# Performance work log

Hardware: AMD Instinct MI355X
Metric: run time of the kernel (lower is better)

## Reference

```python
import jax, jax.numpy as jnp
import numpy as np

B, T, D = 32, 2048, 512


def setup_inputs() -> dict:
    key = jax.random.key(0)
    x = jax.random.normal(key, (B, T, D), dtype=jnp.float32)
    return {"x": x}


def reference(x):
    """DmvCell RNN with aggregations ('mean','var','max').

    Active partials: count, sum, max, mean, sn (Welford M2), var.
    Per step t:
        count += 1
        sum   += x_t
        max    = maximum(max, x_t)
        prev_mean = mean; mean = sum / count
        sn    += (x_t - prev_mean) * (x_t - mean)
        var    = sn / count
        out_t  = concat([mean, var, max])
    Initial states are zeros (Keras default). Returns the full output
    sequence [B, T, 3*D].
    """
    b, t, d = x.shape
    dt = x.dtype

    def step(carry, xt):
        count, s, mx, mean, sn = carry
        count = count + jnp.asarray(1, dt)          # [B,1]
        s = s + xt                                   # [B,D]
        mx = jnp.maximum(mx, xt)                     # [B,D]
        prev_mean = mean
        mean = s / count                             # [B,D]
        sn = sn + (xt - prev_mean) * (xt - mean)     # [B,D]
        var = sn / count                             # [B,D]
        out = jnp.concatenate([mean, var, mx], axis=-1)  # [B,3D]
        return (count, s, mx, mean, sn), out

    init = (
        jnp.zeros((b, 1), dt),   # count
        jnp.zeros((b, d), dt),   # sum
        jnp.zeros((b, d), dt),   # max
        jnp.zeros((b, d), dt),   # mean
        jnp.zeros((b, d), dt),   # sn
    )
    _, ys = jax.lax.scan(step, init, jnp.swapaxes(x, 0, 1))  # ys: [T,B,3D]
    return jnp.swapaxes(ys, 0, 1)  # [B,T,3D]
```

## Files before the change

kernel.cpp:

```cpp
#include <hip/hip_runtime.h>


#define BB 32
#define TT 2048
#define DD 512
#define NCHAIN (BB * DD)

typedef float f32x4 __attribute__((ext_vector_type(4)));

__device__ __forceinline__ float fast_rcp(float x) {
#if __has_builtin(__builtin_amdgcn_rcpf)
    return __builtin_amdgcn_rcpf(x);
#else
    return 1.0f / x;
#endif
}

__device__ __forceinline__ f32x4 vmax4(f32x4 a, f32x4 b) {
#if __has_builtin(__builtin_elementwise_max)
    return __builtin_elementwise_max(a, b);
#else
    f32x4 r;
    r.x = fmaxf(a.x, b.x); r.y = fmaxf(a.y, b.y);
    r.z = fmaxf(a.z, b.z); r.w = fmaxf(a.w, b.w);
    return r;
#endif
}

__device__ __forceinline__ void nts(f32x4 v, float* p) {
#if __has_builtin(__builtin_nontemporal_store)
    __builtin_nontemporal_store(v, (f32x4*)p);
#else
    *(f32x4*)p = v;
#endif
}

struct St1 {
    float n;
    f32x4 s, m2, mx;
};

__device__ __forceinline__ void st1_zero(St1& r) {
    r.n = 0.f;
    r.s = r.m2 = r.mx = (f32x4){0.f, 0.f, 0.f, 0.f};
}

__device__ __forceinline__ void st1_merge(St1& r, float tn, float itn,
                                          f32x4 ts, f32x4 tm, f32x4 tx) {
    if (r.n == 0.f) {
        r.n = tn; r.s = ts; r.m2 = tm; r.mx = tx;
    } else {
        float n     = r.n + tn;
        float irn   = fast_rcp(r.n);
        float scale = r.n * tn * fast_rcp(n);
        f32x4 da = ts * itn - r.s * irn;
        r.m2 += tm + da * da * scale;
        r.s += ts;
        r.mx = vmax4(r.mx, tx);
        r.n = n;
    }
}

template <int NC>
__launch_bounds__(256)
__global__ void dmv_agg_kernel(const float* __restrict__ x,
                               f32x4* __restrict__ ws4) {
    constexpr int CHUNK = TT / NC;
    f32x4* __restrict__ aS  = ws4;
    f32x4* __restrict__ aM2 = ws4 + (size_t)NC * 4096;
    f32x4* __restrict__ aMX = ws4 + 2 * (size_t)NC * 4096;

    const int tid = blockIdx.x * 256 + threadIdx.x;
    const int W   = tid >> 6;
    const int l   = tid & 63;
    const int c   = W & (NC - 1);
    const int b   = W / NC;

    const float* xp = x + ((size_t)(b * TT + c * CHUNK)) * DD + 4 * l;

    f32x4 s0 = {0,0,0,0}, s1 = {0,0,0,0};
    f32x4 q0 = {0,0,0,0}, q1 = {0,0,0,0};
    f32x4 m0 = {0,0,0,0}, m1 = {0,0,0,0};
    #pragma unroll 4
    for (int k = 0; k < CHUNK; ++k) {
        f32x4 a  = *(const f32x4*)(xp + (size_t)k * DD);
        f32x4 b2 = *(const f32x4*)(xp + (size_t)k * DD + 256);
        s0 += a;  q0 += a * a;   m0 = vmax4(m0, a);
        s1 += b2; q1 += b2 * b2; m1 = vmax4(m1, b2);
    }
    const size_t o = (size_t)c * 4096 + (size_t)b * 128 + l;
    const float ic = 1.0f / (float)CHUNK;
    aS[o]       = s0;  aS[o + 64]  = s1;
    aM2[o]      = q0 - s0 * s0 * ic;
    aM2[o + 64] = q1 - s1 * s1 * ic;
    aMX[o]      = m0;  aMX[o + 64] = m1;
}

template <int NC>
__launch_bounds__(512)
__global__ void dmv_scan_split(const float* __restrict__ x,
                               const f32x4* __restrict__ ws4,
                               float* __restrict__ out) {
    constexpr int CHUNK = TT / NC;
    constexpr int GRP   = NC / 4;
    const f32x4* __restrict__ aS  = ws4;
    const f32x4* __restrict__ aM2 = ws4 + (size_t)NC * 4096;
    const f32x4* __restrict__ aMX = ws4 + 2 * (size_t)NC * 4096;

    __shared__ f32x4 part[8][3][64];

    const int tid = threadIdx.x;
    const int w   = tid >> 6;
    const int l   = tid & 63;
    const int h   = w & 1;
    const int cw  = w >> 1;
    const int g   = blockIdx.x & (GRP - 1);
    const int b   = blockIdx.x / GRP;
    const int c0  = g * 4;
    const int c   = c0 + cw;

    constexpr float icf = 1.0f / (float)CHUNK;
    const int hofs = 64 * h;

    St1 q; st1_zero(q);
    for (int j = cw * g; j < (cw + 1) * g; ++j) {
        const size_t oj = (size_t)j * 4096 + (size_t)b * 128 + l + hofs;
        st1_merge(q, (float)CHUNK, icf, aS[oj], aM2[oj], aMX[oj]);
    }
    part[w][0][l] = q.s; part[w][1][l] = q.m2; part[w][2][l] = q.mx;
    __syncthreads();

    St1 r; st1_zero(r);
    if (g > 0) {
        const float qn  = (float)(g * CHUNK);
        const float iqn = fast_rcp(qn);
        #pragma unroll
        for (int qq = 0; qq < 4; ++qq) {
            const int pw = 2 * qq + h;
            st1_merge(r, qn, iqn, part[pw][0][l], part[pw][1][l], part[pw][2][l]);
        }
    }
    for (int j = c0; j < c; ++j) {
        const size_t oj = (size_t)j * 4096 + (size_t)b * 128 + l + hofs;
        st1_merge(r, (float)CHUNK, icf, aS[oj], aM2[oj], aMX[oj]);
    }

    float cnt = r.n;
    f32x4 rs = r.s, rm2 = r.m2, rmx = r.mx;
    f32x4 rmean = {0,0,0,0};
    if (c > 0) rmean = rs * fast_rcp(cnt);

    const float* xp = x   + ((size_t)(b * TT + c * CHUNK)) * DD + h * 256 + 4 * l;
    float*       op = out + ((size_t)(b * TT + c * CHUNK)) * (3 * DD) + h * 256 + 4 * l;

    #pragma unroll 4
    for (int k = 0; k < CHUNK; ++k) {
        f32x4 v = *(const f32x4*)(xp + (size_t)k * DD);
        cnt += 1.f;
        float inv = fast_rcp(cnt);
        rs += v;
        rmx = vmax4(rmx, v);
        f32x4 nm = rs * inv;
        rm2 += (v - rmean) * (v - nm);
        rmean = nm;
        f32x4 var = rm2 * inv;
        float* row = op + (size_t)k * (3 * DD);
        nts(nm,  row);
        nts(var, row + 512);
        nts(rmx, row + 1024);
    }
}

#define FNW 16
#define FCHUNK (TT / FNW)
#define DGRP 64

__launch_bounds__(1024, 1)
__global__ void dmv_scan_fallback(const float* __restrict__ x,
                                  float* __restrict__ out) {
    __shared__ float aggS[FNW][DGRP];
    __shared__ float aggM2[FNW][DGRP];
    __shared__ float aggMX[FNW][DGRP];

    const int tid = threadIdx.x;
    const int w   = tid >> 6;
    const int l   = tid & 63;
    const int b   = blockIdx.x >> 3;
    const int d0  = (blockIdx.x & 7) * DGRP;

    const float* xp = x   + ((size_t)b * TT) * DD + d0 + l
                          + (size_t)(w * FCHUNK) * DD;
    float*       op = out + ((size_t)b * TT) * (3 * DD) + d0 + l
                          + (size_t)(w * FCHUNK) * (3 * DD);

    if (w < FNW - 1) {
        float s = 0.f, ss = 0.f, mx = 0.f;
        #pragma unroll 8
        for (int k = 0; k < FCHUNK; ++k) {
            float xv = xp[(size_t)k * DD];
            s += xv; ss = fmaf(xv, xv, ss); mx = fmaxf(mx, xv);
        }
        aggS[w][l] = s;
        aggM2[w][l] = ss - s * s * (1.0f / FCHUNK);
        aggMX[w][l] = mx;
    }
    __syncthreads();

    float c_n = 0.f, c_s = 0.f, c_m2 = 0.f, c_mx = 0.f;
    for (int j = 0; j < w; ++j) {
        float bs = aggS[j][l], bm2 = aggM2[j][l], bmx = aggMX[j][l];
        if (j == 0) {
            c_n = (float)FCHUNK; c_s = bs; c_m2 = bm2; c_mx = bmx;
        } else {
            float n  = c_n + (float)FCHUNK;
            float da = bs * (1.0f / FCHUNK) - c_s / c_n;
            c_m2 = c_m2 + bm2 + da * da * (c_n * (float)FCHUNK / n);
            c_s += bs; c_mx = fmaxf(c_mx, bmx); c_n = n;
        }
    }

    float cnt = c_n, rs = c_s, rm2 = c_m2, rmx = c_mx;
    float rmean = (w > 0) ? rs / cnt : 0.f;
    #pragma unroll 8
    for (int k = 0; k < FCHUNK; ++k) {
        float xv = xp[(size_t)k * DD];
        cnt += 1.f;
        float inv = fast_rcp(cnt);
        rs += xv; rmx = fmaxf(rmx, xv);
        float nm = rs * inv;
        rm2 += (xv - rmean) * (xv - nm);
        rmean = nm;
        float var = rm2 * inv;
        float* orow = op + (size_t)k * (3 * DD);
        orow[0] = nm; orow[DD] = var; orow[2 * DD] = rmx;
    }
}

template <int NC>
static void launch_2k(const float* x, float* out, void* d_ws, hipStream_t stream) {
    dmv_agg_kernel<NC><<<dim3(8 * NC), dim3(256), 0, stream>>>(x, (f32x4*)d_ws);
    dmv_scan_split<NC><<<dim3(8 * NC), dim3(512), 0, stream>>>(
        x, (const f32x4*)d_ws, out);
}

extern "C" void kernel_launch(void* const* d_in, const int* in_sizes, int n_in,
                              void* d_out, int out_size, void* d_ws, size_t ws_size,
                              hipStream_t stream) {
    (void)in_sizes; (void)n_in; (void)out_size;
    const float* x = (const float*)d_in[0];
    float* out = (float*)d_out;

    const size_t need64 = (size_t)3 * 64 * 4096 * sizeof(f32x4);
    const size_t need32 = (size_t)3 * 32 * 4096 * sizeof(f32x4);

    if (d_ws && ws_size >= need64) {
        launch_2k<64>(x, out, d_ws, stream);
    } else if (d_ws && ws_size >= need32) {
        launch_2k<32>(x, out, d_ws, stream);
    } else {
        dmv_scan_fallback<<<dim3(BB * (DD / DGRP)), dim3(1024), 0, stream>>>(x, out);
    }
}
```

Before: 118.9 us.

## Fuse aggregate and scan kernels using per-batch atomic counters in cooperative launch

```diff
diff --git a/kernel.cpp b/kernel.cpp
--- a/kernel.cpp
+++ b/kernel.cpp
@@ -5,6 +5,7 @@
 #define TT 2048
 #define DD 512
 #define NCHAIN (BB * DD)
+#define NAGG 128
 
 typedef float f32x4 __attribute__((ext_vector_type(4)));
 
@@ -35,10 +36,7 @@
 #endif
 }
 
-struct St1 {
-    float n;
-    f32x4 s, m2, mx;
-};
+struct St1 { float n; f32x4 s, m2, mx; };
 
 __device__ __forceinline__ void st1_zero(St1& r) {
     r.n = 0.f;
@@ -58,6 +56,125 @@
         r.s += ts;
         r.mx = vmax4(r.mx, tx);
         r.n = n;
+    }
+}
+
+template <int NC>
+__launch_bounds__(256, 6)
+__global__ void dmv_fused(const float* __restrict__ x,
+                          f32x4* __restrict__ ws4,
+                          int* __restrict__ cnt,
+                          float* __restrict__ out) {
+    constexpr int CHUNK = TT / NC;
+    constexpr int GRP   = NC / 4;
+    f32x4* __restrict__ aS  = ws4;
+    f32x4* __restrict__ aM2 = ws4 + (size_t)NC * 4096;
+    f32x4* __restrict__ aMX = ws4 + 2 * (size_t)NC * 4096;
+    constexpr float icf = 1.0f / (float)CHUNK;
+
+    __shared__ f32x4 part[4][3][64];
+
+    const int tid = threadIdx.x;
+    const int w   = tid >> 6;
+    const int l   = tid & 63;
+
+    if (blockIdx.x < NAGG) {
+        for (int it = 0; it < 4; ++it) {
+            const int item = blockIdx.x + it * NAGG;
+            const int b  = item >> 4;
+            const int cg = item & 15;
+            const int c  = cg * 4 + w;
+
+            const float* xp = x + ((size_t)(b * TT + c * CHUNK)) * DD + 4 * l;
+            f32x4 s0 = {0,0,0,0}, s1 = {0,0,0,0};
+            f32x4 q0 = {0,0,0,0}, q1 = {0,0,0,0};
+            f32x4 m0 = {0,0,0,0}, m1 = {0,0,0,0};
+            #pragma unroll 4
+            for (int k = 0; k < CHUNK; ++k) {
+                f32x4 a  = *(const f32x4*)(xp + (size_t)k * DD);
+                f32x4 b2 = *(const f32x4*)(xp + (size_t)k * DD + 256);
+                s0 += a;  q0 += a * a;   m0 = vmax4(m0, a);
+                s1 += b2; q1 += b2 * b2; m1 = vmax4(m1, b2);
+            }
+            const size_t o = (size_t)c * 4096 + (size_t)b * 128 + l;
+            aS[o]       = s0;  aS[o + 64]  = s1;
+            aM2[o]      = q0 - s0 * s0 * icf;
+            aM2[o + 64] = q1 - s1 * s1 * icf;
+            aMX[o]      = m0;  aMX[o + 64] = m1;
+
+            __threadfence();
+            __syncthreads();
+            if (tid == 0) {
+                __hip_atomic_fetch_add(&cnt[b], 1, __ATOMIC_RELEASE,
+                                       __HIP_MEMORY_SCOPE_AGENT);
+            }
+            __syncthreads();
+        }
+        return;
+    }
+
+    const int sidx = blockIdx.x - NAGG;
+    const int h    = sidx & 1;
+    const int g    = (sidx >> 1) & (GRP - 1);
+    const int b    = sidx >> 5;
+    const int c0   = g * 4;
+    const int c    = c0 + w;
+    const int hofs = 64 * h;
+
+    if (tid == 0) {
+        while (__hip_atomic_load(&cnt[b], __ATOMIC_RELAXED,
+                                 __HIP_MEMORY_SCOPE_AGENT) < 16) {
+            __builtin_amdgcn_s_sleep(2);
+        }
+    }
+    __syncthreads();
+    __builtin_amdgcn_fence(__ATOMIC_ACQUIRE, "agent");
+
+    St1 q; st1_zero(q);
+    for (int j = w * g; j < (w + 1) * g; ++j) {
+        const size_t oj = (size_t)j * 4096 + (size_t)b * 128 + l + hofs;
+        st1_merge(q, (float)CHUNK, icf, aS[oj], aM2[oj], aMX[oj]);
+    }
+    part[w][0][l] = q.s; part[w][1][l] = q.m2; part[w][2][l] = q.mx;
+    __syncthreads();
+
+    St1 r; st1_zero(r);
+    if (g > 0) {
+        const float qn  = (float)(g * CHUNK);
+        const float iqn = fast_rcp(qn);
+        #pragma unroll
+        for (int qq = 0; qq < 4; ++qq) {
+            st1_merge(r, qn, iqn, part[qq][0][l], part[qq][1][l], part[qq][2][l]);
+        }
+    }
+    for (int j = c0; j < c; ++j) {
+        const size_t oj = (size_t)j * 4096 + (size_t)b * 128 + l + hofs;
+        st1_merge(r, (float)CHUNK, icf, aS[oj], aM2[oj], aMX[oj]);
+    }
+
+    float cnt2 = r.n;
+    f32x4 rs = r.s, rm2 = r.m2, rmx = r.mx;
+    f32x4 rmean = {0,0,0,0};
+    if (c > 0) rmean = rs * fast_rcp(cnt2);
+
+    const float* xp = x   + ((size_t)(b * TT + c * CHUNK)) * DD + h * 256 + 4 * l;
+    float*       op = out + ((size_t)(b * TT + c * CHUNK)) * (3 * DD) + h * 256 + 4 * l;
+
+    #pragma unroll 4
+    for (int k = 0; k < CHUNK; ++k) {
+        f32x4 v = *(const f32x4*)(xp + (size_t)k * DD);
+        cnt2 += 1.f;
+        float inv = fast_rcp(cnt2);
+        rs += v;
+        rmx = vmax4(rmx, v);
+        f32x4 nm = rs * inv;
+        rm2 += (v - rmean) * (v - nm);
+        rmean = nm;
+        f32x4 var = rm2 * inv;
+        float* row = op + (size_t)k * (3 * DD);
+        nts(nm,  row);
+        nts(var, row + 512);
+        nts(rmx, row + 1024);
     }
 }
 
@@ -250,10 +367,23 @@
     const float* x = (const float*)d_in[0];
     float* out = (float*)d_out;
 
-    const size_t need64 = (size_t)3 * 64 * 4096 * sizeof(f32x4);
-    const size_t need32 = (size_t)3 * 32 * 4096 * sizeof(f32x4);
-
-    if (d_ws && ws_size >= need64) {
+    const size_t tabBytes = (size_t)3 * 64 * 4096 * sizeof(f32x4);
+    const size_t needF    = tabBytes + 128;
+    const size_t need64   = tabBytes;
+    const size_t need32   = (size_t)3 * 32 * 4096 * sizeof(f32x4);
+
+    if (d_ws && ws_size >= needF) {
+        f32x4* ws4 = (f32x4*)d_ws;
+        int* cnt = (int*)((char*)d_ws + tabBytes);
+        hipMemsetAsync(cnt, 0, BB * sizeof(int), stream);
+        void* kargs[] = {(void*)&x, (void*)&ws4, (void*)&cnt, (void*)&out};
+        hipError_t e = hipLaunchCooperativeKernel(
+            (const void*)dmv_fused<64>, dim3(NAGG + 1024), dim3(256),
+            kargs, 0, stream);
+        if (e != hipSuccess) {
+            launch_2k<64>(x, out, d_ws, stream);
+        }
+    } else if (d_ws && ws_size >= need64) {
         launch_2k<64>(x, out, d_ws, stream);
     } else if (d_ws && ws_size >= need32) {
         launch_2k<32>(x, out, d_ws, stream);
```

After: 256.2 us. +115.5%, slower.
